# Kernel optimization log

Hardware: AMD Instinct MI355X
Metric: run time of the kernel (lower is better)

The kernel has to match this reference:

```python
import jax, jax.numpy as jnp
import numpy as np

ITER_ROUTING = 3


def squash(t):
    # t: [..., H]
    norm = jnp.sum(t * t, axis=-1)                      # [...]
    scale = norm / (1.0 + norm)
    return scale[..., None] * t / jnp.sqrt(norm)[..., None]


def setup_inputs() -> dict:
    key = jax.random.key(0)
    k1, k2 = jax.random.split(key)
    C, K, H = 1024, 64, 512  # H = 2 * hidden_size, hidden_size = 256
    encoder_output = jax.random.normal(k1, (C, K, H), dtype=jnp.float32)
    # nn.Linear(H, H, bias=False): weight W has shape [H_out, H_in], y = x @ W.T
    W = jax.random.normal(k2, (H, H), dtype=jnp.float32) * (1.0 / np.sqrt(H))
    return {"encoder_output": encoder_output, "W": W}


def reference(encoder_output, W):
    C, K, H = encoder_output.shape
    # Linear projection is identical every iteration in the original loop;
    # compute once (same math, same values).
    x_hat = jnp.einsum('ckh,gh->ckg', encoder_output, W)  # [C, K, H]
    b = jnp.zeros((C, K), dtype=encoder_output.dtype)
    c = None
    for _ in range(ITER_ROUTING):
        d = jax.nn.softmax(b, axis=-1)                    # [C, K]
        c_hat = jnp.sum(x_hat * d[..., None], axis=1)     # [C, H]
        c = squash(c_hat)                                 # [C, H]
        b = b + jnp.einsum('ckh,ch->ck', x_hat, c)        # agreement update
    return c
```

## Files before the change

### kernel.cpp

```cpp
#include <hip/hip_runtime.h>
#include <math.h>


#define KC 64
#define HD 512
#define NT 512

typedef _Float16 half8  __attribute__((ext_vector_type(8)));
typedef _Float16 half4v __attribute__((ext_vector_type(4)));
typedef float    f32x4  __attribute__((ext_vector_type(4)));

__launch_bounds__(256)
__global__ void cast_w_kernel(const float* __restrict__ W, _Float16* __restrict__ Wp) {
    int u    = blockIdx.x * 256 + threadIdx.x;
    int lane = u & 63;
    int j    = (u >> 6) & 3;
    int ks   = (u >> 8) & 1;
    int hs   = (u >> 9) & 7;
    int wv   = (u >> 12) & 7;
    int g  = wv * 64 + j * 16 + (lane & 15);
    int h0 = hs * 64 + ks * 32 + (lane >> 4) * 8;
    const float4* src = reinterpret_cast<const float4*>(W + (size_t)g * HD + h0);
    float4 a = src[0], b = src[1];
    half8 h = { (_Float16)a.x, (_Float16)a.y, (_Float16)a.z, (_Float16)a.w,
                (_Float16)b.x, (_Float16)b.y, (_Float16)b.z, (_Float16)b.w };
    *reinterpret_cast<half8*>(Wp + (size_t)u * 8) = h;
}

__launch_bounds__(NT, 2)
__global__ void routing_kernel(const float* __restrict__ enc,
                               const _Float16* __restrict__ Wp,
                               float* __restrict__ out) {
    __shared__ _Float16 slab[8][8][64][8];
    __shared__ float chatL[HD];
    __shared__ float bpart[2][8][KC];
    __shared__ float redp[2][8];

    const int tid  = threadIdx.x;
    const int lane = tid & 63;
    const int wave = tid >> 6;
    const int l15  = lane & 15, l4 = lane >> 4;
    const int c    = blockIdx.x;
    const float* ebase = enc + (size_t)c * (KC * HD);
    const _Float16* wbase = Wp + ((size_t)wave << 15) + (lane << 3);

    const int r0   = tid >> 4;
    const int c40  = (tid & 15) << 2;
    const int ks_w = c40 >> 5;
    const int l4g  = (c40 >> 3) & 3;
    const int e0w  = c40 & 7;
    const int prow = (l4g * 16 + (r0 & 15)) ^ (l4g << 1);
    const int p0   = (r0 >> 4) * 2 + ks_w;
    const int p1   = p0 + 4;
    const int plane_r = lane ^ ((lane >> 4) << 1);

    half8 bf[2][8];
    auto bload = [&](int hs) {
        #pragma unroll
        for (int q = 0; q < 8; ++q)
            bf[hs & 1][q] = *reinterpret_cast<const half8*>(wbase + hs * 4096 + q * 512);
    };

    float4 ev[8][2];
    #pragma unroll
    for (int hs = 0; hs < 8; ++hs) {
        ev[hs][0] = *reinterpret_cast<const float4*>(ebase + (size_t)r0 * HD + hs * 64 + c40);
        ev[hs][1] = *reinterpret_cast<const float4*>(ebase + (size_t)(r0 + 32) * HD + hs * 64 + c40);
    }
    bload(0);
    #pragma unroll
    for (int hs = 0; hs < 8; ++hs) {
        float4 v0 = ev[hs][0], v1 = ev[hs][1];
        half4v h0 = { (_Float16)v0.x, (_Float16)v0.y, (_Float16)v0.z, (_Float16)v0.w };
        half4v h1 = { (_Float16)v1.x, (_Float16)v1.y, (_Float16)v1.z, (_Float16)v1.w };
        *reinterpret_cast<half4v*>(&slab[hs][p0][prow][e0w]) = h0;
        *reinterpret_cast<half4v*>(&slab[hs][p1][prow][e0w]) = h1;
    }

    f32x4 acc[16];
    #pragma unroll
    for (int i = 0; i < 16; ++i) acc[i] = (f32x4){0.f, 0.f, 0.f, 0.f};

    __syncthreads();

    #pragma unroll
    for (int hs = 0; hs < 8; ++hs) {
        if (hs < 7) bload(hs + 1);
        #pragma unroll
        for (int ks = 0; ks < 2; ++ks) {
            half8 af[4];
            #pragma unroll
            for (int i = 0; i < 4; ++i)
                af[i] = *reinterpret_cast<const half8*>(&slab[hs][i * 2 + ks][plane_r][0]);
            #pragma unroll
            for (int i = 0; i < 4; ++i)
                #pragma unroll
                for (int j = 0; j < 4; ++j)
                    acc[i * 4 + j] = __builtin_amdgcn_mfma_f32_16x16x32_f16(
                        af[i], bf[hs & 1][ks * 4 + j], acc[i * 4 + j], 0, 0, 0);
        }
    }

    float breg = 0.0f;
    float chv[4];

    {
        #pragma unroll
        for (int j = 0; j < 4; ++j) chv[j] = 0.f;
        #pragma unroll
        for (int i = 0; i < 4; ++i)
            #pragma unroll
            for (int r = 0; r < 4; ++r) {
                #pragma unroll
                for (int j = 0; j < 4; ++j)
                    chv[j] += (1.0f / 64.0f) * acc[i * 4 + j][r];
            }
        #pragma unroll
        for (int j = 0; j < 4; ++j) {
            chv[j] += __shfl_xor(chv[j], 16);
            chv[j] += __shfl_xor(chv[j], 32);
        }
        float p = chv[0] * chv[0] + chv[1] * chv[1] + chv[2] * chv[2] + chv[3] * chv[3];
        #pragma unroll
        for (int off = 1; off <= 8; off <<= 1) p += __shfl_xor(p, off);
        if (lane == 0) redp[0][wave] = p;
        #pragma unroll
        for (int i = 0; i < 4; ++i)
            #pragma unroll
            for (int r = 0; r < 4; ++r) {
                float s = acc[i * 4 + 0][r] * chv[0] + acc[i * 4 + 1][r] * chv[1]
                        + acc[i * 4 + 2][r] * chv[2] + acc[i * 4 + 3][r] * chv[3];
                #pragma unroll
                for (int off = 1; off <= 8; off <<= 1) s += __shfl_xor(s, off);
                if (l15 == 0) bpart[0][wave][i * 16 + l4 * 4 + r] = s;
            }
        __syncthreads();
    }

    #pragma unroll
    for (int it = 1; it < 3; ++it) {
        const int rp = (it - 1) & 1, wp = it & 1;
        float n2 = 0.f;
        #pragma unroll
        for (int w = 0; w < 8; ++w) n2 += redp[rp][w];
        float alpha = sqrtf(n2) / (1.0f + n2);
        float dot = 0.f;
        #pragma unroll
        for (int w = 0; w < 8; ++w) dot += bpart[rp][w][lane];
        breg += alpha * dot;
        float m = breg;
        #pragma unroll
        for (int off = 32; off; off >>= 1) m = fmaxf(m, __shfl_xor(m, off));
        float e = expf(breg - m);
        float se = e;
        #pragma unroll
        for (int off = 32; off; off >>= 1) se += __shfl_xor(se, off);
        float dl = e / se;
        #pragma unroll
        for (int j = 0; j < 4; ++j) chv[j] = 0.f;
        #pragma unroll
        for (int i = 0; i < 4; ++i)
            #pragma unroll
            for (int r = 0; r < 4; ++r) {
                float dk = __shfl(dl, i * 16 + l4 * 4 + r);
                #pragma unroll
                for (int j = 0; j < 4; ++j)
                    chv[j] += dk * acc[i * 4 + j][r];
            }
        #pragma unroll
        for (int j = 0; j < 4; ++j) {
            chv[j] += __shfl_xor(chv[j], 16);
            chv[j] += __shfl_xor(chv[j], 32);
        }
        float p = chv[0] * chv[0] + chv[1] * chv[1] + chv[2] * chv[2] + chv[3] * chv[3];
        #pragma unroll
        for (int off = 1; off <= 8; off <<= 1) p += __shfl_xor(p, off);
        if (lane == 0) redp[wp][wave] = p;

        if (it < 2) {
            #pragma unroll
            for (int i = 0; i < 4; ++i)
                #pragma unroll
                for (int r = 0; r < 4; ++r) {
                    float s = acc[i * 4 + 0][r] * chv[0] + acc[i * 4 + 1][r] * chv[1]
                            + acc[i * 4 + 2][r] * chv[2] + acc[i * 4 + 3][r] * chv[3];
                    #pragma unroll
                    for (int off = 1; off <= 8; off <<= 1) s += __shfl_xor(s, off);
                    if (l15 == 0) bpart[wp][wave][i * 16 + l4 * 4 + r] = s;
                }
            __syncthreads();
        } else {
            if (l4 == 0) {
                #pragma unroll
                for (int j = 0; j < 4; ++j)
                    chatL[wave * 64 + j * 16 + l15] = chv[j];
            }
            __syncthreads();
            float n2f = 0.f;
            #pragma unroll
            for (int w = 0; w < 8; ++w) n2f += redp[wp][w];
            float alphaf = sqrtf(n2f) / (1.0f + n2f);
            out[(size_t)c * HD + tid] = alphaf * chatL[tid];
        }
    }
}

extern "C" void kernel_launch(void* const* d_in, const int* in_sizes, int n_in,
                              void* d_out, int out_size, void* d_ws, size_t ws_size,
                              hipStream_t stream) {
    const float* enc = (const float*)d_in[0];
    const float* W   = (const float*)d_in[1];
    float* out       = (float*)d_out;
    _Float16* Wp     = (_Float16*)d_ws;
    (void)in_sizes; (void)n_in; (void)ws_size; (void)out_size;

    cast_w_kernel<<<128, 256, 0, stream>>>(W, Wp);
    routing_kernel<<<1024, NT, 0, stream>>>(enc, Wp, out);
}
```

Baseline: 88.64 us.

## Split fused projection+routing into separate projection and routing kernels via workspace

Splits the single fused kernel into a projection kernel that writes x_hat to workspace as fp16, and a routing kernel that reloads x_hat into LDS and runs the three routing iterations there. This separates the MFMA-heavy phase from the shuffle-heavy routing phase so each kernel can have its own register and LDS profile. In exchange it adds a 64 MB fp16 round trip through global memory plus one extra kernel launch. The original fused kernel is kept as a fallback when the workspace is too small.

```diff
diff --git a/kernel.cpp b/kernel.cpp
--- a/kernel.cpp
+++ b/kernel.cpp
@@ -28,13 +28,10 @@
 }
 
 __launch_bounds__(NT, 2)
-__global__ void routing_kernel(const float* __restrict__ enc,
-                               const _Float16* __restrict__ Wp,
-                               float* __restrict__ out) {
+__global__ void proj_kernel(const float* __restrict__ enc,
+                            const _Float16* __restrict__ Wp,
+                            _Float16* __restrict__ xhat) {
     __shared__ _Float16 slab[8][8][64][8];
-    __shared__ float chatL[HD];
-    __shared__ float bpart[2][8][KC];
-    __shared__ float redp[2][8];
 
     const int tid  = threadIdx.x;
     const int lane = tid & 63;
@@ -101,9 +98,185 @@
         }
     }
 
+    _Float16* xrow = xhat + (size_t)c * (KC * HD);
+    #pragma unroll
+    for (int i = 0; i < 4; ++i) {
+        #pragma unroll
+        for (int j = 0; j < 4; ++j) {
+            f32x4 v = acc[i * 4 + j];
+            const int g  = wave * 64 + j * 16 + l15;
+            const int kb = i * 16 + l4 * 4;
+            #pragma unroll
+            for (int r = 0; r < 4; ++r)
+                xrow[(size_t)(kb + r) * HD + g] = (_Float16)v[r];
+        }
+    }
+}
+
+__launch_bounds__(NT, 2)
+__global__ void route_kernel(const _Float16* __restrict__ xhat,
+                             float* __restrict__ out) {
+    __shared__ _Float16 xh[KC][520];
+    __shared__ float chatL[HD];
+    __shared__ float dL[KC];
+    __shared__ float bdotL[KC];
+    __shared__ float red[8];
+
+    const int tid  = threadIdx.x;
+    const int lane = tid & 63;
+    const int wave = tid >> 6;
+    const int c    = blockIdx.x;
+    const _Float16* xsrc = xhat + (size_t)c * (KC * HD);
+
+    #pragma unroll
+    for (int q = 0; q < 8; ++q) {
+        int flat = tid + q * 512;
+        int row  = flat >> 6;
+        int col  = (flat & 63) << 3;
+        half8 v = *reinterpret_cast<const half8*>(xsrc + (size_t)row * HD + col);
+        *reinterpret_cast<half8*>(&xh[row][col]) = v;
+    }
+    __syncthreads();
+
+    float breg = 0.0f;
+    float alpha = 0.0f;
+
+    #pragma unroll
+    for (int it = 0; it < 3; ++it) {
+        if (it > 0) {
+            breg += bdotL[lane];
+            float m = breg;
+            #pragma unroll
+            for (int off = 32; off; off >>= 1) m = fmaxf(m, __shfl_xor(m, off));
+            float e = expf(breg - m);
+            float se = e;
+            #pragma unroll
+            for (int off = 32; off; off >>= 1) se += __shfl_xor(se, off);
+            if (wave == 0) dL[lane] = e / se;
+            __syncthreads();
+        }
+
+        {
+            float cs = 0.f;
+            if (it == 0) {
+                #pragma unroll 8
+                for (int k = 0; k < KC; ++k) cs += (float)xh[k][tid];
+                cs *= (1.0f / 64.0f);
+            } else {
+                #pragma unroll 8
+                for (int k = 0; k < KC; ++k) cs += dL[k] * (float)xh[k][tid];
+            }
+            chatL[tid] = cs;
+            float p = cs * cs;
+            #pragma unroll
+            for (int off = 32; off; off >>= 1) p += __shfl_xor(p, off);
+            if (lane == 0) red[wave] = p;
+        }
+        __syncthreads();
+        {
+            float n2 = red[0] + red[1] + red[2] + red[3]
+                     + red[4] + red[5] + red[6] + red[7];
+            alpha = sqrtf(n2) / (1.0f + n2);
+        }
+
+        if (it < 2) {
+            float4 cA = *reinterpret_cast<const float4*>(&chatL[lane * 8]);
+            float4 cB = *reinterpret_cast<const float4*>(&chatL[lane * 8 + 4]);
+            #pragma unroll
+            for (int kk = 0; kk < 8; ++kk) {
+                int k = wave * 8 + kk;
+                half8 x = *reinterpret_cast<const half8*>(&xh[k][lane * 8]);
+                float p = (float)x[0] * cA.x + (float)x[1] * cA.y
+                        + (float)x[2] * cA.z + (float)x[3] * cA.w
+                        + (float)x[4] * cB.x + (float)x[5] * cB.y
+                        + (float)x[6] * cB.z + (float)x[7] * cB.w;
+                #pragma unroll
+                for (int off = 32; off; off >>= 1) p += __shfl_xor(p, off);
+                if (lane == 0) bdotL[k] = alpha * p;
+            }
+            __syncthreads();
+        } else {
+            out[(size_t)c * HD + tid] = alpha * chatL[tid];
+        }
+    }
+}
+
+__launch_bounds__(NT, 2)
+__global__ void fused_kernel(const float* __restrict__ enc,
+                             const _Float16* __restrict__ Wp,
+                             float* __restrict__ out) {
+    __shared__ _Float16 slab[8][8][64][8];
+    __shared__ float chatL[HD];
+    __shared__ float bpart[2][8][KC];
+    __shared__ float redp[2][8];
+
+    const int tid  = threadIdx.x;
+    const int lane = tid & 63;
+    const int wave = tid >> 6;
+    const int l15  = lane & 15, l4 = lane >> 4;
+    const int c    = blockIdx.x;
+    const float* ebase = enc + (size_t)c * (KC * HD);
+    const _Float16* wbase = Wp + ((size_t)wave << 15) + (lane << 3);
+
+    const int r0   = tid >> 4;
+    const int c40  = (tid & 15) << 2;
+    const int ks_w = c40 >> 5;
+    const int l4g  = (c40 >> 3) & 3;
+    const int e0w  = c40 & 7;
+    const int prow = (l4g * 16 + (r0 & 15)) ^ (l4g << 1);
+    const int p0   = (r0 >> 4) * 2 + ks_w;
+    const int p1   = p0 + 4;
+    const int plane_r = lane ^ ((lane >> 4) << 1);
+
+    half8 bf[2][8];
+    auto bload = [&](int hs) {
+        #pragma unroll
+        for (int q = 0; q < 8; ++q)
+            bf[hs & 1][q] = *reinterpret_cast<const half8*>(wbase + hs * 4096 + q * 512);
+    };
+
+    float4 ev[8][2];
+    #pragma unroll
+    for (int hs = 0; hs < 8; ++hs) {
+        ev[hs][0] = *reinterpret_cast<const float4*>(ebase + (size_t)r0 * HD + hs * 64 + c40);
+        ev[hs][1] = *reinterpret_cast<const float4*>(ebase + (size_t)(r0 + 32) * HD + hs * 64 + c40);
+    }
+    bload(0);
+    #pragma unroll
+    for (int hs = 0; hs < 8; ++hs) {
+        float4 v0 = ev[hs][0], v1 = ev[hs][1];
+        half4v h0 = { (_Float16)v0.x, (_Float16)v0.y, (_Float16)v0.z, (_Float16)v0.w };
+        half4v h1 = { (_Float16)v1.x, (_Float16)v1.y, (_Float16)v1.z, (_Float16)v1.w };
+        *reinterpret_cast<half4v*>(&slab[hs][p0][prow][e0w]) = h0;
+        *reinterpret_cast<half4v*>(&slab[hs][p1][prow][e0w]) = h1;
+    }
+
+    f32x4 acc[16];
+    #pragma unroll
+    for (int i = 0; i < 16; ++i) acc[i] = (f32x4){0.f, 0.f, 0.f, 0.f};
+
+    __syncthreads();
+
+    #pragma unroll
+    for (int hs = 0; hs < 8; ++hs) {
+        if (hs < 7) bload(hs + 1);
+        #pragma unroll
+        for (int ks = 0; ks < 2; ++ks) {
+            half8 af[4];
+            #pragma unroll
+            for (int i = 0; i < 4; ++i)
+                af[i] = *reinterpret_cast<const half8*>(&slab[hs][i * 2 + ks][plane_r][0]);
+            #pragma unroll
+            for (int i = 0; i < 4; ++i)
+                #pragma unroll
+                for (int j = 0; j < 4; ++j)
+                    acc[i * 4 + j] = __builtin_amdgcn_mfma_f32_16x16x32_f16(
+                        af[i], bf[hs & 1][ks * 4 + j], acc[i * 4 + j], 0, 0, 0);
+        }
+    }
+
     float breg = 0.0f;
     float chv[4];
-
     {
         #pragma unroll
         for (int j = 0; j < 4; ++j) chv[j] = 0.f;
@@ -136,7 +309,6 @@
             }
         __syncthreads();
     }
-
     #pragma unroll
     for (int it = 1; it < 3; ++it) {
         const int rp = (it - 1) & 1, wp = it & 1;
@@ -212,8 +384,17 @@
     const float* W   = (const float*)d_in[1];
     float* out       = (float*)d_out;
     _Float16* Wp     = (_Float16*)d_ws;
-    (void)in_sizes; (void)n_in; (void)ws_size; (void)out_size;
+    (void)in_sizes; (void)n_in; (void)out_size;
+
+    const size_t wp_bytes   = (size_t)512 * 1024;
+    const size_t xhat_bytes = (size_t)1024 * KC * HD * sizeof(_Float16);
 
     cast_w_kernel<<<128, 256, 0, stream>>>(W, Wp);
-    routing_kernel<<<1024, NT, 0, stream>>>(enc, Wp, out);
+    if (ws_size >= wp_bytes + xhat_bytes) {
+        _Float16* xhat = (_Float16*)((char*)d_ws + wp_bytes);
+        proj_kernel<<<1024, NT, 0, stream>>>(enc, Wp, xhat);
+        route_kernel<<<1024, NT, 0, stream>>>(xhat, out);
+    } else {
+        fused_kernel<<<1024, NT, 0, stream>>>(enc, Wp, out);
+    }
 }
```

After: 100.1 us. 12.9% more time.

## Process two capsules per block to reuse W fragments across both

Applied to the files above, without the earlier changes.

Each block now handles two capsules, loading each W fragment once from global and applying it to both capsules' slabs, so W traffic per capsule is halved. The grid shrinks to 512 blocks, shared memory doubles to about 132 KB, and the accumulators double to 128 floats per thread. The higher register and LDS use likely cuts occupancy to one block per CU. The software prefetch of the next W slice is also dropped, so B-load latency is exposed each step.

```diff
diff --git a/kernel.cpp b/kernel.cpp
--- a/kernel.cpp
+++ b/kernel.cpp
@@ -5,6 +5,7 @@
 #define KC 64
 #define HD 512
 #define NT 512
+#define CPB 2
 
 typedef _Float16 half8  __attribute__((ext_vector_type(8)));
 typedef _Float16 half4v __attribute__((ext_vector_type(4)));
@@ -31,17 +32,16 @@
 __global__ void routing_kernel(const float* __restrict__ enc,
                                const _Float16* __restrict__ Wp,
                                float* __restrict__ out) {
-    __shared__ _Float16 slab[8][8][64][8];
-    __shared__ float chatL[HD];
-    __shared__ float bpart[2][8][KC];
-    __shared__ float redp[2][8];
+    __shared__ _Float16 slab[CPB][8][8][64][8];
+    __shared__ float chatL[CPB][HD];
+    __shared__ float bpart[CPB][2][8][KC];
+    __shared__ float redp[CPB][2][8];
 
     const int tid  = threadIdx.x;
     const int lane = tid & 63;
     const int wave = tid >> 6;
     const int l15  = lane & 15, l4 = lane >> 4;
-    const int c    = blockIdx.x;
-    const float* ebase = enc + (size_t)c * (KC * HD);
+    const int c0   = blockIdx.x * CPB;
     const _Float16* wbase = Wp + ((size_t)wave << 15) + (lane << 3);
 
     const int r0   = tid >> 4;
@@ -54,153 +54,172 @@
     const int p1   = p0 + 4;
     const int plane_r = lane ^ ((lane >> 4) << 1);
 
-    half8 bf[2][8];
-    auto bload = [&](int hs) {
+    #pragma unroll
+    for (int cap = 0; cap < CPB; ++cap) {
+        const float* eb = enc + (size_t)(c0 + cap) * (KC * HD);
+        float4 ev[8][2];
+        #pragma unroll
+        for (int hs = 0; hs < 8; ++hs) {
+            ev[hs][0] = *reinterpret_cast<const float4*>(eb + (size_t)r0 * HD + hs * 64 + c40);
+            ev[hs][1] = *reinterpret_cast<const float4*>(eb + (size_t)(r0 + 32) * HD + hs * 64 + c40);
+        }
+        #pragma unroll
+        for (int hs = 0; hs < 8; ++hs) {
+            float4 v0 = ev[hs][0], v1 = ev[hs][1];
+            half4v h0 = { (_Float16)v0.x, (_Float16)v0.y, (_Float16)v0.z, (_Float16)v0.w };
+            half4v h1 = { (_Float16)v1.x, (_Float16)v1.y, (_Float16)v1.z, (_Float16)v1.w };
+            *reinterpret_cast<half4v*>(&slab[cap][hs][p0][prow][e0w]) = h0;
+            *reinterpret_cast<half4v*>(&slab[cap][hs][p1][prow][e0w]) = h1;
+        }
+    }
+
+    f32x4 acc[CPB][16];
+    #pragma unroll
+    for (int cap = 0; cap < CPB; ++cap)
+        #pragma unroll
+        for (int i = 0; i < 16; ++i) acc[cap][i] = (f32x4){0.f, 0.f, 0.f, 0.f};
+
+    __syncthreads();
+
+    #pragma unroll
+    for (int hs = 0; hs < 8; ++hs) {
+        half8 bf[8];
         #pragma unroll
         for (int q = 0; q < 8; ++q)
-            bf[hs & 1][q] = *reinterpret_cast<const half8*>(wbase + hs * 4096 + q * 512);
-    };
-
-    float4 ev[8][2];
-    #pragma unroll
-    for (int hs = 0; hs < 8; ++hs) {
-        ev[hs][0] = *reinterpret_cast<const float4*>(ebase + (size_t)r0 * HD + hs * 64 + c40);
-        ev[hs][1] = *reinterpret_cast<const float4*>(ebase + (size_t)(r0 + 32) * HD + hs * 64 + c40);
-    }
-    bload(0);
-    #pragma unroll
-    for (int hs = 0; hs < 8; ++hs) {
-        float4 v0 = ev[hs][0], v1 = ev[hs][1];
-        half4v h0 = { (_Float16)v0.x, (_Float16)v0.y, (_Float16)v0.z, (_Float16)v0.w };
-        half4v h1 = { (_Float16)v1.x, (_Float16)v1.y, (_Float16)v1.z, (_Float16)v1.w };
-        *reinterpret_cast<half4v*>(&slab[hs][p0][prow][e0w]) = h0;
-        *reinterpret_cast<half4v*>(&slab[hs][p1][prow][e0w]) = h1;
-    }
-
-    f32x4 acc[16];
-    #pragma unroll
-    for (int i = 0; i < 16; ++i) acc[i] = (f32x4){0.f, 0.f, 0.f, 0.f};
-
+            bf[q] = *reinterpret_cast<const half8*>(wbase + hs * 4096 + q * 512);
+        #pragma unroll
+        for (int ks = 0; ks < 2; ++ks) {
+            #pragma unroll
+            for (int cap = 0; cap < CPB; ++cap) {
+                half8 af[4];
+                #pragma unroll
+                for (int i = 0; i < 4; ++i)
+                    af[i] = *reinterpret_cast<const half8*>(&slab[cap][hs][i * 2 + ks][plane_r][0]);
+                #pragma unroll
+                for (int i = 0; i < 4; ++i)
+                    #pragma unroll
+                    for (int j = 0; j < 4; ++j)
+                        acc[cap][i * 4 + j] = __builtin_amdgcn_mfma_f32_16x16x32_f16(
+                            af[i], bf[ks * 4 + j], acc[cap][i * 4 + j], 0, 0, 0);
+            }
+        }
+    }
+
+    float brg[CPB] = {0.f, 0.f};
+    float chv[CPB][4];
+
+    #pragma unroll
+    for (int cap = 0; cap < CPB; ++cap) {
+        #pragma unroll
+        for (int j = 0; j < 4; ++j) chv[cap][j] = 0.f;
+        #pragma unroll
+        for (int i = 0; i < 4; ++i)
+            #pragma unroll
+            for (int r = 0; r < 4; ++r) {
+                #pragma unroll
+                for (int j = 0; j < 4; ++j)
+                    chv[cap][j] += (1.0f / 64.0f) * acc[cap][i * 4 + j][r];
+            }
+        #pragma unroll
+        for (int j = 0; j < 4; ++j) {
+            chv[cap][j] += __shfl_xor(chv[cap][j], 16);
+            chv[cap][j] += __shfl_xor(chv[cap][j], 32);
+        }
+        float p = chv[cap][0] * chv[cap][0] + chv[cap][1] * chv[cap][1]
+                + chv[cap][2] * chv[cap][2] + chv[cap][3] * chv[cap][3];
+        #pragma unroll
+        for (int off = 1; off <= 8; off <<= 1) p += __shfl_xor(p, off);
+        if (lane == 0) redp[cap][0][wave] = p;
+        #pragma unroll
+        for (int i = 0; i < 4; ++i)
+            #pragma unroll
+            for (int r = 0; r < 4; ++r) {
+                float s = acc[cap][i * 4 + 0][r] * chv[cap][0] + acc[cap][i * 4 + 1][r] * chv[cap][1]
+                        + acc[cap][i * 4 + 2][r] * chv[cap][2] + acc[cap][i * 4 + 3][r] * chv[cap][3];
+                #pragma unroll
+                for (int off = 1; off <= 8; off <<= 1) s += __shfl_xor(s, off);
+                if (l15 == 0) bpart[cap][0][wave][i * 16 + l4 * 4 + r] = s;
+            }
+    }
     __syncthreads();
-
-    #pragma unroll
-    for (int hs = 0; hs < 8; ++hs) {
-        if (hs < 7) bload(hs + 1);
-        #pragma unroll
-        for (int ks = 0; ks < 2; ++ks) {
-            half8 af[4];
-            #pragma unroll
-            for (int i = 0; i < 4; ++i)
-                af[i] = *reinterpret_cast<const half8*>(&slab[hs][i * 2 + ks][plane_r][0]);
-            #pragma unroll
-            for (int i = 0; i < 4; ++i)
-                #pragma unroll
-                for (int j = 0; j < 4; ++j)
-                    acc[i * 4 + j] = __builtin_amdgcn_mfma_f32_16x16x32_f16(
-                        af[i], bf[hs & 1][ks * 4 + j], acc[i * 4 + j], 0, 0, 0);
-        }
-    }
-
-    float breg = 0.0f;
-    float chv[4];
-
-    {
-        #pragma unroll
-        for (int j = 0; j < 4; ++j) chv[j] = 0.f;
-        #pragma unroll
-        for (int i = 0; i < 4; ++i)
-            #pragma unroll
-            for (int r = 0; r < 4; ++r) {
-                #pragma unroll
-                for (int j = 0; j < 4; ++j)
-                    chv[j] += (1.0f / 64.0f) * acc[i * 4 + j][r];
-            }
-        #pragma unroll
-        for (int j = 0; j < 4; ++j) {
-            chv[j] += __shfl_xor(chv[j], 16);
-            chv[j] += __shfl_xor(chv[j], 32);
-        }
-        float p = chv[0] * chv[0] + chv[1] * chv[1] + chv[2] * chv[2] + chv[3] * chv[3];
-        #pragma unroll
-        for (int off = 1; off <= 8; off <<= 1) p += __shfl_xor(p, off);
-        if (lane == 0) redp[0][wave] = p;
-        #pragma unroll
-        for (int i = 0; i < 4; ++i)
-            #pragma unroll
-            for (int r = 0; r < 4; ++r) {
-                float s = acc[i * 4 + 0][r] * chv[0] + acc[i * 4 + 1][r] * chv[1]
-                        + acc[i * 4 + 2][r] * chv[2] + acc[i * 4 + 3][r] * chv[3];
-                #pragma unroll
-                for (int off = 1; off <= 8; off <<= 1) s += __shfl_xor(s, off);
-                if (l15 == 0) bpart[0][wave][i * 16 + l4 * 4 + r] = s;
-            }
-        __syncthreads();
-    }
 
     #pragma unroll
     for (int it = 1; it < 3; ++it) {
         const int rp = (it - 1) & 1, wp = it & 1;
-        float n2 = 0.f;
-        #pragma unroll
-        for (int w = 0; w < 8; ++w) n2 += redp[rp][w];
-        float alpha = sqrtf(n2) / (1.0f + n2);
-        float dot = 0.f;
-        #pragma unroll
-        for (int w = 0; w < 8; ++w) dot += bpart[rp][w][lane];
-        breg += alpha * dot;
-        float m = breg;
-        #pragma unroll
-        for (int off = 32; off; off >>= 1) m = fmaxf(m, __shfl_xor(m, off));
-        float e = expf(breg - m);
-        float se = e;
-        #pragma unroll
-        for (int off = 32; off; off >>= 1) se += __shfl_xor(se, off);
-        float dl = e / se;
-        #pragma unroll
-        for (int j = 0; j < 4; ++j) chv[j] = 0.f;
-        #pragma unroll
-        for (int i = 0; i < 4; ++i)
-            #pragma unroll
-            for (int r = 0; r < 4; ++r) {
-                float dk = __shfl(dl, i * 16 + l4 * 4 + r);
-                #pragma unroll
-                for (int j = 0; j < 4; ++j)
-                    chv[j] += dk * acc[i * 4 + j][r];
-            }
-        #pragma unroll
-        for (int j = 0; j < 4; ++j) {
-            chv[j] += __shfl_xor(chv[j], 16);
-            chv[j] += __shfl_xor(chv[j], 32);
-        }
-        float p = chv[0] * chv[0] + chv[1] * chv[1] + chv[2] * chv[2] + chv[3] * chv[3];
-        #pragma unroll
-        for (int off = 1; off <= 8; off <<= 1) p += __shfl_xor(p, off);
-        if (lane == 0) redp[wp][wave] = p;
+        #pragma unroll
+        for (int cap = 0; cap < CPB; ++cap) {
+            float n2 = 0.f;
+            #pragma unroll
+            for (int w = 0; w < 8; ++w) n2 += redp[cap][rp][w];
+            float alpha = sqrtf(n2) / (1.0f + n2);
+            float dot = 0.f;
+            #pragma unroll
+            for (int w = 0; w < 8; ++w) dot += bpart[cap][rp][w][lane];
+            brg[cap] += alpha * dot;
+            float m = brg[cap];
+            #pragma unroll
+            for (int off = 32; off; off >>= 1) m = fmaxf(m, __shfl_xor(m, off));
+            float e = expf(brg[cap] - m);
+            float se = e;
+            #pragma unroll
+            for (int off = 32; off; off >>= 1) se += __shfl_xor(se, off);
+            float dl = e / se;
+            #pragma unroll
+            for (int j = 0; j < 4; ++j) chv[cap][j] = 0.f;
+            #pragma unroll
+            for (int i = 0; i < 4; ++i)
+                #pragma unroll
+                for (int r = 0; r < 4; ++r) {
+                    float dk = __shfl(dl, i * 16 + l4 * 4 + r);
+                    #pragma unroll
+                    for (int j = 0; j < 4; ++j)
+                        chv[cap][j] += dk * acc[cap][i * 4 + j][r];
+                }
+            #pragma unroll
+            for (int j = 0; j < 4; ++j) {
+                chv[cap][j] += __shfl_xor(chv[cap][j], 16);
+                chv[cap][j] += __shfl_xor(chv[cap][j], 32);
+            }
+            float p = chv[cap][0] * chv[cap][0] + chv[cap][1] * chv[cap][1]
+                    + chv[cap][2] * chv[cap][2] + chv[cap][3] * chv[cap][3];
+            #pragma unroll
+            for (int off = 1; off <= 8; off <<= 1) p += __shfl_xor(p, off);
+            if (lane == 0) redp[cap][wp][wave] = p;
+        }
 
         if (it < 2) {
             #pragma unroll
-            for (int i = 0; i < 4; ++i)
-                #pragma unroll
-                for (int r = 0; r < 4; ++r) {
-                    float s = acc[i * 4 + 0][r] * chv[0] + acc[i * 4 + 1][r] * chv[1]
-                            + acc[i * 4 + 2][r] * chv[2] + acc[i * 4 + 3][r] * chv[3];
-                    #pragma unroll
-                    for (int off = 1; off <= 8; off <<= 1) s += __shfl_xor(s, off);
-                    if (l15 == 0) bpart[wp][wave][i * 16 + l4 * 4 + r] = s;
-                }
+            for (int cap = 0; cap < CPB; ++cap) {
+                #pragma unroll
+                for (int i = 0; i < 4; ++i)
+                    #pragma unroll
+                    for (int r = 0; r < 4; ++r) {
+                        float s = acc[cap][i * 4 + 0][r] * chv[cap][0] + acc[cap][i * 4 + 1][r] * chv[cap][1]
+                                + acc[cap][i * 4 + 2][r] * chv[cap][2] + acc[cap][i * 4 + 3][r] * chv[cap][3];
+                        #pragma unroll
+                        for (int off = 1; off <= 8; off <<= 1) s += __shfl_xor(s, off);
+                        if (l15 == 0) bpart[cap][wp][wave][i * 16 + l4 * 4 + r] = s;
+                    }
+            }
             __syncthreads();
         } else {
-            if (l4 == 0) {
-                #pragma unroll
-                for (int j = 0; j < 4; ++j)
-                    chatL[wave * 64 + j * 16 + l15] = chv[j];
+            #pragma unroll
+            for (int cap = 0; cap < CPB; ++cap) {
+                if (l4 == 0) {
+                    #pragma unroll
+                    for (int j = 0; j < 4; ++j)
+                        chatL[cap][wave * 64 + j * 16 + l15] = chv[cap][j];
+                }
             }
             __syncthreads();
-            float n2f = 0.f;
-            #pragma unroll
-            for (int w = 0; w < 8; ++w) n2f += redp[wp][w];
-            float alphaf = sqrtf(n2f) / (1.0f + n2f);
-            out[(size_t)c * HD + tid] = alphaf * chatL[tid];
+            #pragma unroll
+            for (int cap = 0; cap < CPB; ++cap) {
+                float n2f = 0.f;
+                #pragma unroll
+                for (int w = 0; w < 8; ++w) n2f += redp[cap][wp][w];
+                float alphaf = sqrtf(n2f) / (1.0f + n2f);
+                out[(size_t)(c0 + cap) * HD + tid] = alphaf * chatL[cap][tid];
+            }
         }
     }
 }
@@ -215,5 +234,5 @@
     (void)in_sizes; (void)n_in; (void)ws_size; (void)out_size;
 
     cast_w_kernel<<<128, 256, 0, stream>>>(W, Wp);
-    routing_kernel<<<1024, NT, 0, stream>>>(enc, Wp, out);
+    routing_kernel<<<1024 / CPB, NT, 0, stream>>>(enc, Wp, out);
 }
```

Result: faster. 82.26 us (-7.2%).
